# Performance work log

Hardware: AMD Instinct MI355X
Metric: run time of the kernel (lower is better)

The kernel has to match this reference:

```python
import jax, jax.numpy as jnp
import numpy as np

N_NODES = 50000
N_EDGES = 1250000
VOCAB = 50000
EMBED = 64
HIDDEN = 64
NUM_REL = 3
N_CLASSES = 2
N_GRAPHS = 512


def setup_inputs() -> dict:
    key = jax.random.key(0)
    ks = jax.random.split(key, 12)
    x = jax.random.randint(ks[0], (N_NODES,), 0, VOCAB, dtype=jnp.int32)
    edge_index = jax.random.randint(ks[1], (2, N_EDGES), 0, N_NODES, dtype=jnp.int32)
    edge_type = jax.random.randint(ks[2], (N_EDGES,), 0, NUM_REL, dtype=jnp.int32)
    batch = jnp.sort(jax.random.randint(ks[3], (N_NODES,), 0, N_GRAPHS, dtype=jnp.int32))
    s = 0.05
    emb = jax.random.normal(ks[4], (VOCAB, EMBED), jnp.float32) * s
    w1_rel = jax.random.normal(ks[5], (NUM_REL, EMBED, HIDDEN), jnp.float32) * s
    w1_root = jax.random.normal(ks[6], (EMBED, HIDDEN), jnp.float32) * s
    b1 = jnp.zeros((HIDDEN,), jnp.float32)
    w2_rel = jax.random.normal(ks[7], (NUM_REL, HIDDEN, HIDDEN), jnp.float32) * s
    w2_root = jax.random.normal(ks[8], (HIDDEN, HIDDEN), jnp.float32) * s
    b2 = jnp.zeros((HIDDEN,), jnp.float32)
    lin_w = jax.random.normal(ks[9], (HIDDEN, N_CLASSES), jnp.float32) * s
    lin_b = jnp.zeros((N_CLASSES,), jnp.float32)
    return {"x": x, "edge_index": edge_index, "edge_type": edge_type, "batch": batch,
            "emb": emb, "w1_rel": w1_rel, "w1_root": w1_root, "b1": b1,
            "w2_rel": w2_rel, "w2_root": w2_root, "b2": b2,
            "lin_w": lin_w, "lin_b": lin_b}


def rgcn_conv(h, src, dst, edge_type, w_rel, w_root, bias):
    # PyG RGCNConv: out = h @ W_root + bias + sum_r mean-aggregated (h_src @ W_r)
    out = h @ w_root + bias
    h_src = h[src]  # [E, F] gather
    for r in range(NUM_REL):
        mask = (edge_type == r).astype(h.dtype)  # [E]
        m = (h_src @ w_rel[r]) * mask[:, None]   # [E, H]
        s = jax.ops.segment_sum(m, dst, num_segments=N_NODES)
        cnt = jax.ops.segment_sum(mask, dst, num_segments=N_NODES)
        out = out + s / jnp.maximum(cnt, 1.0)[:, None]
    return out


def reference(x, edge_index, edge_type, batch, emb, w1_rel, w1_root, b1,
              w2_rel, w2_root, b2, lin_w, lin_b):
    src, dst = edge_index[0], edge_index[1]
    emb_eff = emb.at[0].set(0.0)  # padding_idx=0
    h = emb_eff[x]  # [N, EMBED]
    h = jax.nn.relu(rgcn_conv(h, src, dst, edge_type, w1_rel, w1_root, b1))
    h = jax.nn.relu(rgcn_conv(h, src, dst, edge_type, w2_rel, w2_root, b2))
    # global mean pool over graphs
    sums = jax.ops.segment_sum(h, batch, num_segments=N_GRAPHS)
    cnt = jax.ops.segment_sum(jnp.ones((h.shape[0],), h.dtype), batch, num_segments=N_GRAPHS)
    pooled = sums / jnp.maximum(cnt, 1.0)[:, None]  # [G, HIDDEN]
    return pooled @ lin_w + lin_b  # [G, N_CLASSES]
```

## Files before the change

### kernel.cpp

```cpp
#include <hip/hip_runtime.h>

#define CHUNK 2048

__global__ __launch_bounds__(256) void embed_count_kernel(
    const int* __restrict__ x, const float* __restrict__ emb, float* __restrict__ h0,
    const int* __restrict__ ei, int* __restrict__ pcount,
    int n_nodes, int n_edges, int n_bkt, int embed_blocks)
{
    __shared__ int cnt[512];
    int t = threadIdx.x;
    if ((int)blockIdx.x < embed_blocks) {
        int tt = blockIdx.x * 256 + t;
        if (tt < n_nodes * 16) {
            int n = tt >> 4, q = tt & 15;
            int xv = x[n];
            float4 v = {0.f, 0.f, 0.f, 0.f};
            if (xv != 0) v = *(const float4*)(emb + (size_t)xv * 64 + q * 4);
            *(float4*)(h0 + (size_t)n * 64 + q * 4) = v;
        }
        return;
    }
    int jb = blockIdx.x - embed_blocks;
    for (int b = t; b < 512; b += 256) cnt[b] = 0;
    __syncthreads();
    int base = jb * CHUNK;
#pragma unroll
    for (int i = 0; i < CHUNK / 256; ++i) {
        int e = base + i * 256 + t;
        if (e < n_edges) atomicAdd(&cnt[ei[n_edges + e] >> 7], 1);
    }
    __syncthreads();
    for (int b = t; b < n_bkt; b += 256) pcount[jb * n_bkt + b] = cnt[b];
}

__global__ __launch_bounds__(256) void colscan_kernel(
    const int* __restrict__ pcount, int* __restrict__ pre,
    int* __restrict__ totals, int* __restrict__ rowstartR,
    const int* __restrict__ batch, const float* __restrict__ linb,
    float* __restrict__ inv_cnt, float* __restrict__ outg,
    int n_chk, int n_bkt, int n_edges, int n_nodes, int n_graphs)
{
    __shared__ int ps[256];
    int b = blockIdx.x, t = threadIdx.x;
    if (b >= n_bkt) {
        int g = (b - n_bkt) * 256 + t;
        if (g < n_graphs) {
            int lo = 0, hi = n_nodes;
            while (lo < hi) { int mid = (lo + hi) >> 1; if (batch[mid] < g) lo = mid + 1; else hi = mid; }
            int s = lo;
            lo = 0; hi = n_nodes;
            while (lo < hi) { int mid = (lo + hi) >> 1; if (batch[mid] < g + 1) lo = mid + 1; else hi = mid; }
            inv_cnt[g] = 1.f / (float)max(lo - s, 1);
            outg[2 * g + 0] = linb[0];
            outg[2 * g + 1] = linb[1];
        }
        return;
    }
    if (b == 0 && t == 0) rowstartR[4 * n_nodes] = n_edges;
    int v[4], s = 0;
#pragma unroll
    for (int i = 0; i < 4; ++i) {
        int jj = t * 4 + i;
        v[i] = (jj < n_chk) ? pcount[jj * n_bkt + b] : 0;
        s += v[i];
    }
    ps[t] = s;
    __syncthreads();
    for (int o = 1; o < 256; o <<= 1) {
        int u = (t >= o) ? ps[t - o] : 0;
        __syncthreads();
        ps[t] += u;
        __syncthreads();
    }
    int run = (t > 0) ? ps[t - 1] : 0;
#pragma unroll
    for (int i = 0; i < 4; ++i) {
        int jj = t * 4 + i;
        if (jj < n_chk) pre[jj * n_bkt + b] = run;
        run += v[i];
    }
    if (t == 255) totals[b] = run;
}

__global__ __launch_bounds__(256) void scatter_kernel(
    const int* __restrict__ ei, const int* __restrict__ et,
    const int* __restrict__ pre, const int* __restrict__ totals,
    int* __restrict__ esort, int* __restrict__ bucket_start,
    int n_edges, int n_bkt)
{
    __shared__ int bs[512], fill2[512], ps[256];
    int t = threadIdx.x, j = blockIdx.x;
    int a0 = (2 * t < n_bkt) ? totals[2 * t] : 0;
    int a1 = (2 * t + 1 < n_bkt) ? totals[2 * t + 1] : 0;
    ps[t] = a0 + a1;
    __syncthreads();
    for (int o = 1; o < 256; o <<= 1) {
        int u = (t >= o) ? ps[t - o] : 0;
        __syncthreads();
        ps[t] += u;
        __syncthreads();
    }
    int basex = (t > 0) ? ps[t - 1] : 0;
    bs[2 * t] = basex;
    bs[2 * t + 1] = basex + a0;
    fill2[t] = 0; fill2[t + 256] = 0;
    __syncthreads();
    if (j == 0) {
        for (int b = t; b < n_bkt; b += 256) bucket_start[b] = bs[b];
        if (t == 0) bucket_start[n_bkt] = n_edges;
    }
    for (int b = t; b < n_bkt; b += 256) bs[b] += pre[j * n_bkt + b];
    __syncthreads();
    int base = j * CHUNK;
#pragma unroll
    for (int i = 0; i < CHUNK / 256; ++i) {
        int e = base + i * 256 + t;
        if (e < n_edges) {
            int s = ei[e], d = ei[n_edges + e], r = et[e];
            int b = d >> 7;
            int pos = bs[b] + atomicAdd(&fill2[b], 1);
            esort[pos] = s | (r << 16) | ((d & 127) << 18);
        }
    }
}

__global__ __launch_bounds__(256) void bucket_sort_kernel(
    const int* __restrict__ bucket_start, int* __restrict__ esort,
    int* __restrict__ scratch, int* __restrict__ rowstartR, int n_nodes)
{
    __shared__ int cnt[512], off[512], fill[512], ps[256];
    int t = threadIdx.x, b = blockIdx.x;
    int s = bucket_start[b], e = bucket_start[b + 1];
    cnt[t] = 0; cnt[t + 256] = 0; fill[t] = 0; fill[t + 256] = 0;
    __syncthreads();
    int* scr = scratch + (size_t)b * 8192;
    for (int i = s + t; i < e; i += 256) {
        int p = esort[i];
        scr[i - s] = p;
        atomicAdd(&cnt[(p >> 16) & 0x1FF], 1);
    }
    __syncthreads();
    int a0 = cnt[2 * t], a1 = cnt[2 * t + 1];
    ps[t] = a0 + a1;
    __syncthreads();
    for (int o = 1; o < 256; o <<= 1) {
        int v = (t >= o) ? ps[t - o] : 0;
        __syncthreads();
        ps[t] += v;
        __syncthreads();
    }
    int basex = (t > 0) ? ps[t - 1] : 0;
    off[2 * t] = basex;
    off[2 * t + 1] = basex + a0;
    __syncthreads();
    int d0 = b * 128 + (2 * t >> 2);
    if (d0 < n_nodes) rowstartR[b * 512 + 2 * t] = s + off[2 * t];
    int d1 = b * 128 + ((2 * t + 1) >> 2);
    if (d1 < n_nodes) rowstartR[b * 512 + 2 * t + 1] = s + off[2 * t + 1];
    __syncthreads();
    for (int i = s + t; i < e; i += 256) {
        int p = scr[i - s];
        int bin = (p >> 16) & 0x1FF;
        int pos = s + off[bin] + atomicAdd(&fill[bin], 1);
        esort[pos] = p;
    }
}

__global__ __launch_bounds__(256) void agg_kernel(
    const float* __restrict__ hin, const int* __restrict__ rowstartR,
    const int* __restrict__ esort, float* __restrict__ means, int n_nodes)
{
    int wid = (blockIdx.x * 256 + threadIdx.x) >> 6;
    int lane = threadIdx.x & 63;
    if (wid >= n_nodes) return;
    int q = lane >> 4;
    int c = lane & 15;
    int4 rs = *(const int4*)(rowstartR + wid * 4);
    int s = rs.x, e = rs.w;

    float4 a0 = {0.f,0.f,0.f,0.f}, a1 = {0.f,0.f,0.f,0.f}, a2 = {0.f,0.f,0.f,0.f};

    int i = s + 4 * q;
    for (; i + 4 <= e; i += 16) {
        int p0 = esort[i], p1 = esort[i + 1], p2 = esort[i + 2], p3 = esort[i + 3];
        float4 v0 = *(const float4*)(hin + (size_t)(p0 & 0xFFFF) * 64 + c * 4);
        float4 v1 = *(const float4*)(hin + (size_t)(p1 & 0xFFFF) * 64 + c * 4);
        float4 v2 = *(const float4*)(hin + (size_t)(p2 & 0xFFFF) * 64 + c * 4);
        float4 v3 = *(const float4*)(hin + (size_t)(p3 & 0xFFFF) * 64 + c * 4);
#pragma unroll
        for (int m = 0; m < 4; ++m) {
            int p = m == 0 ? p0 : m == 1 ? p1 : m == 2 ? p2 : p3;
            float4 v = m == 0 ? v0 : m == 1 ? v1 : m == 2 ? v2 : v3;
            int r = (p >> 16) & 3;
            float m0 = (r == 0) ? 1.f : 0.f;
            float m1 = (r == 1) ? 1.f : 0.f;
            float m2 = (r == 2) ? 1.f : 0.f;
            a0.x = fmaf(m0, v.x, a0.x); a0.y = fmaf(m0, v.y, a0.y);
            a0.z = fmaf(m0, v.z, a0.z); a0.w = fmaf(m0, v.w, a0.w);
            a1.x = fmaf(m1, v.x, a1.x); a1.y = fmaf(m1, v.y, a1.y);
            a1.z = fmaf(m1, v.z, a1.z); a1.w = fmaf(m1, v.w, a1.w);
            a2.x = fmaf(m2, v.x, a2.x); a2.y = fmaf(m2, v.y, a2.y);
            a2.z = fmaf(m2, v.z, a2.z); a2.w = fmaf(m2, v.w, a2.w);
        }
    }
#pragma unroll
    for (int m = 0; m < 3; ++m) {
        int ii = i + m;
        if (ii < e) {
            int p = esort[ii];
            float4 v = *(const float4*)(hin + (size_t)(p & 0xFFFF) * 64 + c * 4);
            int r = (p >> 16) & 3;
            float m0 = (r == 0) ? 1.f : 0.f;
            float m1 = (r == 1) ? 1.f : 0.f;
            float m2 = (r == 2) ? 1.f : 0.f;
            a0.x = fmaf(m0, v.x, a0.x); a0.y = fmaf(m0, v.y, a0.y);
            a0.z = fmaf(m0, v.z, a0.z); a0.w = fmaf(m0, v.w, a0.w);
            a1.x = fmaf(m1, v.x, a1.x); a1.y = fmaf(m1, v.y, a1.y);
            a1.z = fmaf(m1, v.z, a1.z); a1.w = fmaf(m1, v.w, a1.w);
            a2.x = fmaf(m2, v.x, a2.x); a2.y = fmaf(m2, v.y, a2.y);
            a2.z = fmaf(m2, v.z, a2.z); a2.w = fmaf(m2, v.w, a2.w);
        }
    }
#pragma unroll
    for (int off = 16; off < 64; off <<= 1) {
        a0.x += __shfl_xor(a0.x, off); a0.y += __shfl_xor(a0.y, off);
        a0.z += __shfl_xor(a0.z, off); a0.w += __shfl_xor(a0.w, off);
        a1.x += __shfl_xor(a1.x, off); a1.y += __shfl_xor(a1.y, off);
        a1.z += __shfl_xor(a1.z, off); a1.w += __shfl_xor(a1.w, off);
        a2.x += __shfl_xor(a2.x, off); a2.y += __shfl_xor(a2.y, off);
        a2.z += __shfl_xor(a2.z, off); a2.w += __shfl_xor(a2.w, off);
    }
    if (q < 3) {
        int cnt = (q == 0) ? (rs.y - rs.x) : (q == 1) ? (rs.z - rs.y) : (rs.w - rs.z);
        float4 a = (q == 0) ? a0 : (q == 1) ? a1 : a2;
        float inv = 1.f / (float)max(cnt, 1);
        float4 m = {a.x * inv, a.y * inv, a.z * inv, a.w * inv};
        *(float4*)(means + (size_t)wid * 192 + q * 64 + c * 4) = m;
    }
}

__global__ __launch_bounds__(256) void transform_kernel(
    const float* __restrict__ hin, const float* __restrict__ means,
    const float* __restrict__ wroot, const float* __restrict__ wrel,
    const float* __restrict__ bias, float* __restrict__ hout,
    const int* __restrict__ batch, const float* __restrict__ linw,
    const float* __restrict__ inv_cnt, float* __restrict__ outg,
    int n_nodes, int do_pool)
{
    __shared__ float wsh[2][4096];
    __shared__ float gacc[64][2];
    int t = threadIdx.x;
    int gt = blockIdx.x * 256 + t;
    int g = gt >> 4, q = gt & 15;
    int n0 = g * 4;
    bool active = (n0 < n_nodes);

    {
        const float4* sp = (const float4*)wroot;
        float4* d = (float4*)wsh[0];
#pragma unroll
        for (int i = 0; i < 4; ++i) d[t + i * 256] = sp[t + i * 256];
    }

    float4 acc[4];
    float4 b = {0.f, 0.f, 0.f, 0.f};
    if (active) b = *(const float4*)(bias + q * 4);
#pragma unroll
    for (int i = 0; i < 4; ++i) acc[i] = b;

    const float* hv = hin + (size_t)n0 * 64;
    const float* mv = means + (size_t)n0 * 192;

    for (int s = 0; s < 4; ++s) {
        __syncthreads();
        if (s < 3) {
            const float4* sp = (const float4*)wrel + (size_t)s * 1024;
            float4* d = (float4*)wsh[(s + 1) & 1];
#pragma unroll
            for (int i = 0; i < 4; ++i) d[t + i * 256] = sp[t + i * 256];
        }
        const float* vbase = (s == 0) ? hv : (mv + (s - 1) * 64);
        int vstride = (s == 0) ? 64 : 192;
        const float* wbuf = wsh[s & 1];
        if (active) {
#pragma unroll 4
            for (int k4 = 0; k4 < 16; ++k4) {
                float4 v[4];
#pragma unroll
                for (int i = 0; i < 4; ++i)
                    v[i] = *(const float4*)(vbase + i * vstride + k4 * 4);
#pragma unroll
                for (int kk = 0; kk < 4; ++kk) {
                    float4 w = *(const float4*)(wbuf + (k4 * 4 + kk) * 64 + q * 4);
#pragma unroll
                    for (int i = 0; i < 4; ++i) {
                        float sv = kk == 0 ? v[i].x : kk == 1 ? v[i].y : kk == 2 ? v[i].z : v[i].w;
                        acc[i].x = fmaf(sv, w.x, acc[i].x);
                        acc[i].y = fmaf(sv, w.y, acc[i].y);
                        acc[i].z = fmaf(sv, w.z, acc[i].z);
                        acc[i].w = fmaf(sv, w.w, acc[i].w);
                    }
                }
            }
        }
    }
    if (!do_pool) {
        if (active) {
            float* o = hout + (size_t)n0 * 64 + q * 4;
#pragma unroll
            for (int i = 0; i < 4; ++i) {
                float4 r = {fmaxf(acc[i].x, 0.f), fmaxf(acc[i].y, 0.f),
                            fmaxf(acc[i].z, 0.f), fmaxf(acc[i].w, 0.f)};
                *(float4*)(o + i * 64) = r;
            }
        }
    } else {
        if (t < 64) { gacc[t][0] = 0.f; gacc[t][1] = 0.f; }
        __syncthreads();
        int nbase = blockIdx.x * 64;
        int gmin = batch[min(nbase, n_nodes - 1)];
        if (active) {
            float4 lwA = *(const float4*)(linw + q * 8);
            float4 lwB = *(const float4*)(linw + q * 8 + 4);
            float d0[4], d1[4];
#pragma unroll
            for (int i = 0; i < 4; ++i) {
                float4 r = {fmaxf(acc[i].x, 0.f), fmaxf(acc[i].y, 0.f),
                            fmaxf(acc[i].z, 0.f), fmaxf(acc[i].w, 0.f)};
                d0[i] = r.x * lwA.x + r.y * lwA.z + r.z * lwB.x + r.w * lwB.z;
                d1[i] = r.x * lwA.y + r.y * lwA.w + r.z * lwB.y + r.w * lwB.w;
            }
#pragma unroll
            for (int off = 1; off < 16; off <<= 1) {
#pragma unroll
                for (int i = 0; i < 4; ++i) {
                    d0[i] += __shfl_xor(d0[i], off);
                    d1[i] += __shfl_xor(d1[i], off);
                }
            }
            if (q == 0) {
#pragma unroll
                for (int i = 0; i < 4; ++i) {
                    int n = n0 + i;
                    if (n < n_nodes) {
                        int gg = batch[n];
                        float ic = inv_cnt[gg];
                        int idx = gg - gmin;
                        if (idx < 64) {
                            atomicAdd(&gacc[idx][0], d0[i] * ic);
                            atomicAdd(&gacc[idx][1], d1[i] * ic);
                        } else {
                            atomicAdd(&outg[2 * gg + 0], d0[i] * ic);
                            atomicAdd(&outg[2 * gg + 1], d1[i] * ic);
                        }
                    }
                }
            }
        }
        __syncthreads();
        if (t < 64) {
            float v0 = gacc[t][0], v1 = gacc[t][1];
            if (v0 != 0.f || v1 != 0.f) {
                atomicAdd(&outg[2 * (gmin + t) + 0], v0);
                atomicAdd(&outg[2 * (gmin + t) + 1], v1);
            }
        }
    }
}

extern "C" void kernel_launch(void* const* d_in, const int* in_sizes, int n_in,
                              void* d_out, int out_size, void* d_ws, size_t ws_size,
                              hipStream_t stream)
{
    const int*   x      = (const int*)d_in[0];
    const int*   ei     = (const int*)d_in[1];
    const int*   et     = (const int*)d_in[2];
    const int*   batch  = (const int*)d_in[3];
    const float* emb    = (const float*)d_in[4];
    const float* w1rel  = (const float*)d_in[5];
    const float* w1root = (const float*)d_in[6];
    const float* b1     = (const float*)d_in[7];
    const float* w2rel  = (const float*)d_in[8];
    const float* w2root = (const float*)d_in[9];
    const float* b2     = (const float*)d_in[10];
    const float* linw   = (const float*)d_in[11];
    const float* linb   = (const float*)d_in[12];
    float* out = (float*)d_out;

    const int N = in_sizes[0];
    const int E = in_sizes[2];
    const int G = out_size / 2;
    const int NBKT = (N + 127) >> 7;
    const int NCHK = (E + CHUNK - 1) / CHUNK;

    float* hA        = (float*)d_ws;
    float* hB        = hA + (size_t)N * 64;
    float* means     = hB + (size_t)N * 64;
    int*   esort     = (int*)(means + (size_t)N * 192);
    int*   rowstartR = esort + E;
    int*   bucket_start = rowstartR + 4 * N + 4;
    int*   totals    = bucket_start + NBKT + 1;
    float* inv_cnt   = (float*)(totals + NBKT);
    int*   scratch   = (int*)means;
    int*   pcount    = (int*)means + 4 * 1024 * 1024;
    int*   pre       = (int*)means + 5 * 1024 * 1024;

    int embedBlocks = (N * 16 + 255) / 256;
    embed_count_kernel<<<embedBlocks + NCHK, 256, 0, stream>>>(
        x, emb, hA, ei, pcount, N, E, NBKT, embedBlocks);
    int gBlocks = (G + 255) / 256;
    colscan_kernel<<<NBKT + gBlocks, 256, 0, stream>>>(
        pcount, pre, totals, rowstartR, batch, linb, inv_cnt, out,
        NCHK, NBKT, E, N, G);
    scatter_kernel<<<NCHK, 256, 0, stream>>>(ei, et, pre, totals, esort, bucket_start, E, NBKT);
    bucket_sort_kernel<<<NBKT, 256, 0, stream>>>(bucket_start, esort, scratch, rowstartR, N);

    int aggBlocks = (N * 64 + 255) / 256;
    int tfBlocks  = ((N + 3) / 4 * 16 + 255) / 256;
    agg_kernel<<<aggBlocks, 256, 0, stream>>>(hA, rowstartR, esort, means, N);
    transform_kernel<<<tfBlocks, 256, 0, stream>>>(
        hA, means, w1root, w1rel, b1, hB, batch, linw, inv_cnt, out, N, 0);
    agg_kernel<<<aggBlocks, 256, 0, stream>>>(hB, rowstartR, esort, means, N);
    transform_kernel<<<tfBlocks, 256, 0, stream>>>(
        hB, means, w2root, w2rel, b2, hA, batch, linw, inv_cnt, out, N, 1);
}
```

Before: 308.5 us.

## Pipeline transform weights via LDS direct loads and simplify aggregation masks

The transform kernel now splits each weight matrix into half-size LDS chunks. Chunks are staged with global_load_lds, double-buffered over eight sub-stages, and the first node-feature float4 of the next stage is prefetched, with launch bounds raised for occupancy. Separately, the aggregation kernel reads edge indices with nontemporal loads. It also computes the relation-0 sum as the total minus the relation-1 and relation-2 sums, saving FMAs per edge. The aim is to hide weight-load latency and trim ALU work, at the cost of more barriers, slightly different float rounding and reliance on compiler waitcnt handling for the LDS direct loads.

```diff
diff --git a/kernel.cpp b/kernel.cpp
--- a/kernel.cpp
+++ b/kernel.cpp
@@ -182,7 +182,10 @@
 
     int i = s + 4 * q;
     for (; i + 4 <= e; i += 16) {
-        int p0 = esort[i], p1 = esort[i + 1], p2 = esort[i + 2], p3 = esort[i + 3];
+        int p0 = __builtin_nontemporal_load(esort + i);
+        int p1 = __builtin_nontemporal_load(esort + i + 1);
+        int p2 = __builtin_nontemporal_load(esort + i + 2);
+        int p3 = __builtin_nontemporal_load(esort + i + 3);
         float4 v0 = *(const float4*)(hin + (size_t)(p0 & 0xFFFF) * 64 + c * 4);
         float4 v1 = *(const float4*)(hin + (size_t)(p1 & 0xFFFF) * 64 + c * 4);
         float4 v2 = *(const float4*)(hin + (size_t)(p2 & 0xFFFF) * 64 + c * 4);
@@ -192,11 +195,9 @@
             int p = m == 0 ? p0 : m == 1 ? p1 : m == 2 ? p2 : p3;
             float4 v = m == 0 ? v0 : m == 1 ? v1 : m == 2 ? v2 : v3;
             int r = (p >> 16) & 3;
-            float m0 = (r == 0) ? 1.f : 0.f;
-            float m1 = (r == 1) ? 1.f : 0.f;
-            float m2 = (r == 2) ? 1.f : 0.f;
-            a0.x = fmaf(m0, v.x, a0.x); a0.y = fmaf(m0, v.y, a0.y);
-            a0.z = fmaf(m0, v.z, a0.z); a0.w = fmaf(m0, v.w, a0.w);
+            float m1 = (float)(r & 1);
+            float m2 = (float)(r >> 1);
+            a0.x += v.x; a0.y += v.y; a0.z += v.z; a0.w += v.w;
             a1.x = fmaf(m1, v.x, a1.x); a1.y = fmaf(m1, v.y, a1.y);
             a1.z = fmaf(m1, v.z, a1.z); a1.w = fmaf(m1, v.w, a1.w);
             a2.x = fmaf(m2, v.x, a2.x); a2.y = fmaf(m2, v.y, a2.y);
@@ -207,20 +208,20 @@
     for (int m = 0; m < 3; ++m) {
         int ii = i + m;
         if (ii < e) {
-            int p = esort[ii];
+            int p = __builtin_nontemporal_load(esort + ii);
             float4 v = *(const float4*)(hin + (size_t)(p & 0xFFFF) * 64 + c * 4);
             int r = (p >> 16) & 3;
-            float m0 = (r == 0) ? 1.f : 0.f;
-            float m1 = (r == 1) ? 1.f : 0.f;
-            float m2 = (r == 2) ? 1.f : 0.f;
-            a0.x = fmaf(m0, v.x, a0.x); a0.y = fmaf(m0, v.y, a0.y);
-            a0.z = fmaf(m0, v.z, a0.z); a0.w = fmaf(m0, v.w, a0.w);
+            float m1 = (float)(r & 1);
+            float m2 = (float)(r >> 1);
+            a0.x += v.x; a0.y += v.y; a0.z += v.z; a0.w += v.w;
             a1.x = fmaf(m1, v.x, a1.x); a1.y = fmaf(m1, v.y, a1.y);
             a1.z = fmaf(m1, v.z, a1.z); a1.w = fmaf(m1, v.w, a1.w);
             a2.x = fmaf(m2, v.x, a2.x); a2.y = fmaf(m2, v.y, a2.y);
             a2.z = fmaf(m2, v.z, a2.z); a2.w = fmaf(m2, v.w, a2.w);
         }
     }
+    a0.x -= a1.x + a2.x; a0.y -= a1.y + a2.y;
+    a0.z -= a1.z + a2.z; a0.w -= a1.w + a2.w;
 #pragma unroll
     for (int off = 16; off < 64; off <<= 1) {
         a0.x += __shfl_xor(a0.x, off); a0.y += __shfl_xor(a0.y, off);
@@ -239,7 +240,15 @@
     }
 }
 
-__global__ __launch_bounds__(256) void transform_kernel(
+__device__ __forceinline__ void stage16(const float* gsrc, float* ldst)
+{
+    __builtin_amdgcn_global_load_lds(
+        (const __attribute__((address_space(1))) unsigned int*)gsrc,
+        (__attribute__((address_space(3))) unsigned int*)ldst,
+        16, 0, 0);
+}
+
+__global__ __launch_bounds__(256, 4) void transform_kernel(
     const float* __restrict__ hin, const float* __restrict__ means,
     const float* __restrict__ wroot, const float* __restrict__ wrel,
     const float* __restrict__ bias, float* __restrict__ hout,
@@ -247,7 +256,7 @@
     const float* __restrict__ inv_cnt, float* __restrict__ outg,
     int n_nodes, int do_pool)
 {
-    __shared__ float wsh[2][4096];
+    __shared__ float wsh[2][2048];
     __shared__ float gacc[64][2];
     int t = threadIdx.x;
     int gt = blockIdx.x * 256 + t;
@@ -255,40 +264,61 @@
     int n0 = g * 4;
     bool active = (n0 < n_nodes);
 
+    stage16(wroot + t * 4,        wsh[0] + t * 4);
+    stage16(wroot + 1024 + t * 4, wsh[0] + 1024 + t * 4);
+
+    float4 acc[4];
     {
-        const float4* sp = (const float4*)wroot;
-        float4* d = (float4*)wsh[0];
-#pragma unroll
-        for (int i = 0; i < 4; ++i) d[t + i * 256] = sp[t + i * 256];
-    }
-
-    float4 acc[4];
-    float4 b = {0.f, 0.f, 0.f, 0.f};
-    if (active) b = *(const float4*)(bias + q * 4);
-#pragma unroll
-    for (int i = 0; i < 4; ++i) acc[i] = b;
+        float4 b = {0.f, 0.f, 0.f, 0.f};
+        if (active) b = *(const float4*)(bias + q * 4);
+#pragma unroll
+        for (int i = 0; i < 4; ++i) acc[i] = b;
+    }
 
     const float* hv = hin + (size_t)n0 * 64;
     const float* mv = means + (size_t)n0 * 192;
 
-    for (int s = 0; s < 4; ++s) {
-        __syncthreads();
-        if (s < 3) {
-            const float4* sp = (const float4*)wrel + (size_t)s * 1024;
-            float4* d = (float4*)wsh[(s + 1) & 1];
-#pragma unroll
-            for (int i = 0; i < 4; ++i) d[t + i * 256] = sp[t + i * 256];
-        }
-        const float* vbase = (s == 0) ? hv : (mv + (s - 1) * 64);
-        int vstride = (s == 0) ? 64 : 192;
-        const float* wbuf = wsh[s & 1];
+    float4 vpre[4];
+    if (active) {
+#pragma unroll
+        for (int i = 0; i < 4; ++i) vpre[i] = *(const float4*)(hv + i * 64);
+    }
+
+    for (int ss = 0; ss < 8; ++ss) {
+        int p  = ss >> 1;
+        int kb = (ss & 1) * 32;
+        const float* vb = (p == 0) ? hv : (mv + (p - 1) * 64);
+        int vst = (p == 0) ? 64 : 192;
+        int pn  = (ss + 1) >> 1;
+        int kbn = ((ss + 1) & 1) * 32;
+        const float* vbn = (pn == 0) ? hv : (mv + (pn - 1) * 64);
+        int vstn = (pn == 0) ? 64 : 192;
+
+        __syncthreads();
+        if (ss < 7) {
+            const float* wsrc = (ss + 1 < 2) ? (wroot + (size_t)(ss + 1) * 2048)
+                                             : (wrel + (size_t)(ss - 1) * 2048);
+            float* d = wsh[(ss + 1) & 1];
+            stage16(wsrc + t * 4,        d + t * 4);
+            stage16(wsrc + 1024 + t * 4, d + 1024 + t * 4);
+        }
+        const float* wbuf = wsh[ss & 1];
         if (active) {
-#pragma unroll 4
-            for (int k4 = 0; k4 < 16; ++k4) {
+            float4 v0c[4];
+#pragma unroll
+            for (int i = 0; i < 4; ++i) v0c[i] = vpre[i];
+            if (ss < 7) {
+#pragma unroll
+                for (int i = 0; i < 4; ++i)
+                    vpre[i] = *(const float4*)(vbn + i * vstn + kbn);
+            }
+#pragma unroll
+            for (int k4 = 0; k4 < 8; ++k4) {
                 float4 v[4];
 #pragma unroll
                 for (int i = 0; i < 4; ++i)
-                    v[i] = *(const float4*)(vbase + i * vstride + k4 * 4);
+                    v[i] = (k4 == 0) ? v0c[i]
+                                     : *(const float4*)(vb + i * vst + kb + k4 * 4);
 #pragma unroll
                 for (int kk = 0; kk < 4; ++kk) {
                     float4 w = *(const float4*)(wbuf + (k4 * 4 + kk) * 64 + q * 4);
```

After: 309.5 us. Within noise of the previous version (+0.3%).

## Transpose partial counts, drop bucket-sort scratch copy, stage weights via LDS DMA

Applied to the files above, without the earlier changes.

Partial bucket counts are now stored bucket-major, so the column scan reads contiguous memory. The bucket sort reads from the scattered array and writes to a separate output buffer instead of copying into scratch first, which removes one global write and read per edge. The transform kernel moves to 128-thread blocks, streams the weights in 32-row halves through a smaller double buffer, and fills that buffer with global_load_lds DMA. The smaller LDS footprint is meant to allow more resident blocks, at the cost of more barriers and an extra workspace region for the second sort buffer.

```diff
diff --git a/kernel.cpp b/kernel.cpp
--- a/kernel.cpp
+++ b/kernel.cpp
@@ -5,7 +5,7 @@
 __global__ __launch_bounds__(256) void embed_count_kernel(
     const int* __restrict__ x, const float* __restrict__ emb, float* __restrict__ h0,
     const int* __restrict__ ei, int* __restrict__ pcount,
-    int n_nodes, int n_edges, int n_bkt, int embed_blocks)
+    int n_nodes, int n_edges, int n_bkt, int n_chk, int embed_blocks)
 {
     __shared__ int cnt[512];
     int t = threadIdx.x;
@@ -30,7 +30,7 @@
         if (e < n_edges) atomicAdd(&cnt[ei[n_edges + e] >> 7], 1);
     }
     __syncthreads();
-    for (int b = t; b < n_bkt; b += 256) pcount[jb * n_bkt + b] = cnt[b];
+    for (int b = t; b < n_bkt; b += 256) pcount[b * n_chk + jb] = cnt[b];
 }
 
 __global__ __launch_bounds__(256) void colscan_kernel(
@@ -61,7 +61,7 @@
 #pragma unroll
     for (int i = 0; i < 4; ++i) {
         int jj = t * 4 + i;
-        v[i] = (jj < n_chk) ? pcount[jj * n_bkt + b] : 0;
+        v[i] = (jj < n_chk) ? pcount[b * n_chk + jj] : 0;
         s += v[i];
     }
     ps[t] = s;
@@ -125,20 +125,16 @@
 }
 
 __global__ __launch_bounds__(256) void bucket_sort_kernel(
-    const int* __restrict__ bucket_start, int* __restrict__ esort,
-    int* __restrict__ scratch, int* __restrict__ rowstartR, int n_nodes)
+    const int* __restrict__ bucket_start, const int* __restrict__ esort_in,
+    int* __restrict__ esort_out, int* __restrict__ rowstartR, int n_nodes)
 {
     __shared__ int cnt[512], off[512], fill[512], ps[256];
     int t = threadIdx.x, b = blockIdx.x;
     int s = bucket_start[b], e = bucket_start[b + 1];
     cnt[t] = 0; cnt[t + 256] = 0; fill[t] = 0; fill[t + 256] = 0;
     __syncthreads();
-    int* scr = scratch + (size_t)b * 8192;
-    for (int i = s + t; i < e; i += 256) {
-        int p = esort[i];
-        scr[i - s] = p;
-        atomicAdd(&cnt[(p >> 16) & 0x1FF], 1);
-    }
+    for (int i = s + t; i < e; i += 256)
+        atomicAdd(&cnt[(esort_in[i] >> 16) & 0x1FF], 1);
     __syncthreads();
     int a0 = cnt[2 * t], a1 = cnt[2 * t + 1];
     ps[t] = a0 + a1;
@@ -159,10 +155,10 @@
     if (d1 < n_nodes) rowstartR[b * 512 + 2 * t + 1] = s + off[2 * t + 1];
     __syncthreads();
     for (int i = s + t; i < e; i += 256) {
-        int p = scr[i - s];
+        int p = esort_in[i];
         int bin = (p >> 16) & 0x1FF;
         int pos = s + off[bin] + atomicAdd(&fill[bin], 1);
-        esort[pos] = p;
+        esort_out[pos] = p;
     }
 }
 
@@ -239,7 +235,15 @@
     }
 }
 
-__global__ __launch_bounds__(256) void transform_kernel(
+__device__ __forceinline__ void stage16(const float* gsrc, float* ldst)
+{
+    __builtin_amdgcn_global_load_lds(
+        (const __attribute__((address_space(1))) unsigned int*)gsrc,
+        (__attribute__((address_space(3))) unsigned int*)ldst,
+        16, 0, 0);
+}
+
+__global__ __launch_bounds__(128, 4) void transform_kernel(
     const float* __restrict__ hin, const float* __restrict__ means,
     const float* __restrict__ wroot, const float* __restrict__ wrel,
     const float* __restrict__ bias, float* __restrict__ hout,
@@ -247,48 +251,51 @@
     const float* __restrict__ inv_cnt, float* __restrict__ outg,
     int n_nodes, int do_pool)
 {
-    __shared__ float wsh[2][4096];
+    __shared__ float wsh[2][2048];
     __shared__ float gacc[64][2];
     int t = threadIdx.x;
-    int gt = blockIdx.x * 256 + t;
+    int gt = blockIdx.x * 128 + t;
     int g = gt >> 4, q = gt & 15;
     int n0 = g * 4;
     bool active = (n0 < n_nodes);
 
+#pragma unroll
+    for (int i = 0; i < 4; ++i)
+        stage16(wroot + i * 512 + t * 4, wsh[0] + i * 512 + t * 4);
+
+    float4 acc[4];
     {
-        const float4* sp = (const float4*)wroot;
-        float4* d = (float4*)wsh[0];
-#pragma unroll
-        for (int i = 0; i < 4; ++i) d[t + i * 256] = sp[t + i * 256];
-    }
-
-    float4 acc[4];
-    float4 b = {0.f, 0.f, 0.f, 0.f};
-    if (active) b = *(const float4*)(bias + q * 4);
-#pragma unroll
-    for (int i = 0; i < 4; ++i) acc[i] = b;
+        float4 b = {0.f, 0.f, 0.f, 0.f};
+        if (active) b = *(const float4*)(bias + q * 4);
+#pragma unroll
+        for (int i = 0; i < 4; ++i) acc[i] = b;
+    }
 
     const float* hv = hin + (size_t)n0 * 64;
     const float* mv = means + (size_t)n0 * 192;
 
-    for (int s = 0; s < 4; ++s) {
-        __syncthreads();
-        if (s < 3) {
-            const float4* sp = (const float4*)wrel + (size_t)s * 1024;
-            float4* d = (float4*)wsh[(s + 1) & 1];
-#pragma unroll
-            for (int i = 0; i < 4; ++i) d[t + i * 256] = sp[t + i * 256];
-        }
-        const float* vbase = (s == 0) ? hv : (mv + (s - 1) * 64);
-        int vstride = (s == 0) ? 64 : 192;
-        const float* wbuf = wsh[s & 1];
+    for (int ss = 0; ss < 8; ++ss) {
+        __syncthreads();
+        if (ss < 7) {
+            const float* wsrc = (ss + 1 < 2) ? (wroot + (size_t)(ss + 1) * 2048)
+                                             : (wrel + (size_t)(ss - 1) * 2048);
+            float* d = wsh[(ss + 1) & 1];
+#pragma unroll
+            for (int i = 0; i < 4; ++i)
+                stage16(wsrc + i * 512 + t * 4, d + i * 512 + t * 4);
+        }
+        int p  = ss >> 1;
+        int kb = (ss & 1) * 32;
+        const float* vb = ((p == 0) ? hv : (mv + (p - 1) * 64)) + kb;
+        int vst = (p == 0) ? 64 : 192;
+        const float* wbuf = wsh[ss & 1];
         if (active) {
-#pragma unroll 4
-            for (int k4 = 0; k4 < 16; ++k4) {
+#pragma unroll
+            for (int k4 = 0; k4 < 8; ++k4) {
                 float4 v[4];
 #pragma unroll
                 for (int i = 0; i < 4; ++i)
-                    v[i] = *(const float4*)(vbase + i * vstride + k4 * 4);
+                    v[i] = *(const float4*)(vb + i * vst + k4 * 4);
 #pragma unroll
                 for (int kk = 0; kk < 4; ++kk) {
                     float4 w = *(const float4*)(wbuf + (k4 * 4 + kk) * 64 + q * 4);
@@ -317,7 +324,7 @@
     } else {
         if (t < 64) { gacc[t][0] = 0.f; gacc[t][1] = 0.f; }
         __syncthreads();
-        int nbase = blockIdx.x * 64;
+        int nbase = blockIdx.x * 32;
         int gmin = batch[min(nbase, n_nodes - 1)];
         if (active) {
             float4 lwA = *(const float4*)(linw + q * 8);
@@ -401,26 +408,26 @@
     int*   bucket_start = rowstartR + 4 * N + 4;
     int*   totals    = bucket_start + NBKT + 1;
     float* inv_cnt   = (float*)(totals + NBKT);
-    int*   scratch   = (int*)means;
+    int*   esort2    = (int*)(inv_cnt + G);
     int*   pcount    = (int*)means + 4 * 1024 * 1024;
     int*   pre       = (int*)means + 5 * 1024 * 1024;
 
     int embedBlocks = (N * 16 + 255) / 256;
     embed_count_kernel<<<embedBlocks + NCHK, 256, 0, stream>>>(
-        x, emb, hA, ei, pcount, N, E, NBKT, embedBlocks);
+        x, emb, hA, ei, pcount, N, E, NBKT, NCHK, embedBlocks);
     int gBlocks = (G + 255) / 256;
     colscan_kernel<<<NBKT + gBlocks, 256, 0, stream>>>(
         pcount, pre, totals, rowstartR, batch, linb, inv_cnt, out,
         NCHK, NBKT, E, N, G);
     scatter_kernel<<<NCHK, 256, 0, stream>>>(ei, et, pre, totals, esort, bucket_start, E, NBKT);
-    bucket_sort_kernel<<<NBKT, 256, 0, stream>>>(bucket_start, esort, scratch, rowstartR, N);
+    bucket_sort_kernel<<<NBKT, 256, 0, stream>>>(bucket_start, esort, esort2, rowstartR, N);
 
     int aggBlocks = (N * 64 + 255) / 256;
-    int tfBlocks  = ((N + 3) / 4 * 16 + 255) / 256;
-    agg_kernel<<<aggBlocks, 256, 0, stream>>>(hA, rowstartR, esort, means, N);
-    transform_kernel<<<tfBlocks, 256, 0, stream>>>(
+    int tfBlocks  = (N + 31) / 32;
+    agg_kernel<<<aggBlocks, 256, 0, stream>>>(hA, rowstartR, esort2, means, N);
+    transform_kernel<<<tfBlocks, 128, 0, stream>>>(
         hA, means, w1root, w1rel, b1, hB, batch, linw, inv_cnt, out, N, 0);
-    agg_kernel<<<aggBlocks, 256, 0, stream>>>(hB, rowstartR, esort, means, N);
-    transform_kernel<<<tfBlocks, 256, 0, stream>>>(
+    agg_kernel<<<aggBlocks, 256, 0, stream>>>(hB, rowstartR, esort2, means, N);
+    transform_kernel<<<tfBlocks, 128, 0, stream>>>(
         hB, means, w2root, w2rel, b2, hA, batch, linw, inv_cnt, out, N, 1);
 }
```

Result: no change. 308.2 us (-0.1%).
